# Optimization experiments

Measured on AMD Instinct MI355X. Metric: run time of the kernel, lower is better.

## Reference

```python
import jax, jax.numpy as jnp
import numpy as np

HEADS, DIM_HEAD = 8, 75            # Attention defaults in source
SCALE = DIM_HEAD ** -0.5
NUM_FOURIER = 64
PATCH = 4


def scale_norm(x, g, eps=1e-5):
    n = jnp.maximum(jnp.linalg.norm(x, axis=-1, keepdims=True), eps)
    return x / n * g


def attention(x, ctx, mask, wq, wkv, wo, bo):
    b, nq, _ = x.shape
    q = (x @ wq).reshape(b, nq, HEADS, DIM_HEAD)
    k, v = jnp.split(ctx @ wkv, 2, axis=-1)
    k = k.reshape(b, -1, HEADS, DIM_HEAD)
    v = v.reshape(b, -1, HEADS, DIM_HEAD)
    sim = jnp.einsum('bihd,bjhd->bhij', q, k) * SCALE
    if mask is not None:
        sim = jnp.where(mask[:, None, None, :], sim, -jnp.finfo(sim.dtype).max)
    a = jax.nn.softmax(sim, axis=-1)
    out = jnp.einsum('bhij,bjhd->bihd', a, v).reshape(b, nq, HEADS * DIM_HEAD)
    return out @ wo + bo


def feedforward(x, w1, b1, w2, b2):
    return jax.nn.gelu(x @ w1 + b1, approximate=False) @ w2 + b2


def fourier_encode(x, num_encodings):
    xu = x[..., None]
    scales = (2.0 ** jnp.arange(num_encodings)).astype(x.dtype)
    xs = xu / scales
    return jnp.concatenate([jnp.sin(xs), jnp.cos(xs), xu], axis=-1)


def sparsify(x, threshold=0.3):
    # x: (b, h, w, nt, c) patched volume. Fixed max_len = h*w*nt; stable sort
    # compacts kept voxels to the front in row-major (y,x,t) order, matching
    # torch.where ordering. Padded slots are zeroed and masked out.
    b, h, w, nt, c = x.shape
    N = h * w * nt
    mask = (jnp.abs(jnp.max(x, axis=-1)) > threshold).reshape(b, N)
    ys, xs, ts = jnp.meshgrid(jnp.arange(h), jnp.arange(w), jnp.arange(nt), indexing='ij')
    pos = jnp.stack([2.0 * ys / h - 1.0, 2.0 * xs / w - 1.0, 2.0 * ts / nt - 1.0], -1)
    pos = pos.reshape(N, 3).astype(x.dtype)
    order = jnp.argsort((~mask).astype(jnp.int32), axis=1)  # jax sort is stable
    mask_s = jnp.take_along_axis(mask, order, axis=1)
    pos_s = pos[order] * mask_s[..., None]
    vals_s = jnp.take_along_axis(x.reshape(b, N, c), order[..., None], axis=1) * mask_s[..., None]
    return pos_s, vals_s, mask_s


def _forward(input, latents, pos_emb,
             ca_g, ca_ctx_g, ca_q, ca_kv, ca_ow, ca_ob,
             cf_g, cf_w1, cf_b1, cf_w2, cf_b2,
             la_g, la_q, la_kv, la_ow, la_ob,
             lf_g, lf_w1, lf_b1, lf_w2, lf_b2,
             logits_w, logits_b):
    num_tbins = input.shape[0]
    x = jnp.transpose(input, (1, 3, 4, 0, 2))  # b h w t c
    b, H, W, t, c = x.shape
    p = PATCH
    x = x.reshape(b, H // p, p, W // p, p, t, c)
    x = jnp.transpose(x, (0, 1, 3, 5, 2, 4, 6)).reshape(b, H // p, W // p, t, p * p * c)
    pos, vals, mask = sparsify(x)
    enc = fourier_encode(pos, NUM_FOURIER)           # (b, N, 3, 2*nf+1)
    enc = enc.reshape(enc.shape[0], enc.shape[1], -1)
    data = jnp.concatenate([vals, enc], axis=-1)     # (b, N, input_dim)
    data = jax.lax.stop_gradient(data)               # torch builds it under no_grad
    lat = jnp.broadcast_to((latents + pos_emb)[None], (b,) + latents.shape)
    depth = ca_g.shape[0]
    for d in range(depth):
        lat = attention(scale_norm(lat, ca_g[d]), scale_norm(data, ca_ctx_g[d]), mask,
                        ca_q[d], ca_kv[d], ca_ow[d], ca_ob[d]) + lat
        lat = feedforward(scale_norm(lat, cf_g[d]), cf_w1[d], cf_b1[d], cf_w2[d], cf_b2[d]) + lat
        xn = scale_norm(lat, la_g[d])
        lat = attention(xn, xn, None, la_q[d], la_kv[d], la_ow[d], la_ob[d]) + lat
        lat = feedforward(scale_norm(lat, lf_g[d]), lf_w1[d], lf_b1[d], lf_w2[d], lf_b2[d]) + lat
    out = lat @ logits_w + logits_b                  # (b, num_latents, oc)
    n = out.shape[1] // num_tbins
    out = out.reshape(b, n, num_tbins, out.shape[-1])
    return jnp.transpose(out, (2, 0, 1, 3))          # (t, b, n, oc)


def setup_inputs() -> dict:
    key = jax.random.key(0)
    ks = jax.random.split(key, 16)
    D, LD, ID, IN, FF, NL, OC = 5, 512, 435, 600, 2048, 128, 64
    def rn(k, shape, scale=0.02):
        return jax.random.normal(k, shape, jnp.float32) * scale
    return {
        'input': jax.random.normal(ks[0], (8, 4, 3, 128, 128), jnp.float32),
        'latents': rn(ks[1], (NL, LD), 1.0),
        'pos_emb': rn(ks[2], (NL, LD), 1.0),
        'ca_g': jnp.ones((D,), jnp.float32),
        'ca_ctx_g': jnp.ones((D,), jnp.float32),
        'ca_q': rn(ks[3], (D, LD, IN)),
        'ca_kv': rn(ks[4], (D, ID, 2 * IN)),
        'ca_ow': rn(ks[5], (D, IN, LD)),
        'ca_ob': jnp.zeros((D, LD), jnp.float32),
        'cf_g': jnp.ones((D,), jnp.float32),
        'cf_w1': rn(ks[6], (D, LD, FF)),
        'cf_b1': jnp.zeros((D, FF), jnp.float32),
        'cf_w2': rn(ks[7], (D, FF, LD)),
        'cf_b2': jnp.zeros((D, LD), jnp.float32),
        'la_g': jnp.ones((D,), jnp.float32),
        'la_q': rn(ks[8], (D, LD, IN)),
        'la_kv': rn(ks[9], (D, LD, 2 * IN)),
        'la_ow': rn(ks[10], (D, IN, LD)),
        'la_ob': jnp.zeros((D, LD), jnp.float32),
        'lf_g': jnp.ones((D,), jnp.float32),
        'lf_w1': rn(ks[11], (D, LD, FF)),
        'lf_b1': jnp.zeros((D, FF), jnp.float32),
        'lf_w2': rn(ks[12], (D, FF, LD)),
        'lf_b2': jnp.zeros((D, LD), jnp.float32),
        'logits_w': rn(ks[13], (LD, OC)),
        'logits_b': jnp.zeros((OC,), jnp.float32),
    }


def reference(input, latents, pos_emb,
              ca_g, ca_ctx_g, ca_q, ca_kv, ca_ow, ca_ob,
              cf_g, cf_w1, cf_b1, cf_w2, cf_b2,
              la_g, la_q, la_kv, la_ow, la_ob,
              lf_g, lf_w1, lf_b1, lf_w2, lf_b2,
              logits_w, logits_b):
    return _forward(input, latents, pos_emb,
                    ca_g, ca_ctx_g, ca_q, ca_kv, ca_ow, ca_ob,
                    cf_g, cf_w1, cf_b1, cf_w2, cf_b2,
                    la_g, la_q, la_kv, la_ow, la_ob,
                    lf_g, lf_w1, lf_b1, lf_w2, lf_b2,
                    logits_w, logits_b)
```

## Files before the change

kernel.cpp:

```cpp
#include <hip/hip_runtime.h>
#include <math.h>

typedef unsigned short u16;
typedef long long ll;
typedef __attribute__((ext_vector_type(8))) short short8;
typedef __attribute__((ext_vector_type(4))) float f32x4;

#define TBINS 8
#define BATCH 4
#define CIN 3
#define WIMG 128
#define PC 48
#define NVOX 8192
#define ID 435
#define IDP 448
#define LD 512
#define INNER 600
#define INNERP 608
#define FFD 2048
#define NL 128
#define OC 64
#define DEPTH 5
#define HEADS 8
#define DH 75
#define DHP 96
#define BK 32
#define NCH 16
#define FCH 512
#define FKT 64

static __device__ __forceinline__ u16 f2bf(float f) {
    unsigned x = __float_as_uint(f);
    unsigned r = (x + 0x7fffu + ((x >> 16) & 1u)) >> 16;
    return (u16)r;
}
static __device__ __forceinline__ float bf2f(u16 v) {
    return __uint_as_float(((unsigned)v) << 16);
}
static __device__ __forceinline__ void gload_lds16(const u16* g, u16* l) {
    __builtin_amdgcn_global_load_lds(
        (const __attribute__((address_space(1))) unsigned int*)g,
        (__attribute__((address_space(3))) unsigned int*)l, 16, 0, 0);
}

__global__ __launch_bounds__(256) void mask_kernel(const float* __restrict__ input,
                                                   unsigned char* __restrict__ mask) {
    int idx = blockIdx.x * 256 + threadIdx.x;
    if (idx >= BATCH * NVOX) return;
    int b = idx >> 13, i = idx & (NVOX - 1);
    int tt = i & 7, wx = (i >> 3) & 31, hy = i >> 8;
    float mx = -3.4e38f;
    for (int ch = 0; ch < PC; ++ch) {
        int py = ch / 12, px = (ch / 3) & 3, cc = ch % 3;
        float v = input[((size_t)((tt * BATCH + b) * CIN + cc) << 14) +
                        (hy * 4 + py) * WIMG + (wx * 4 + px)];
        mx = fmaxf(mx, v);
    }
    mask[idx] = (fabsf(mx) > 0.3f) ? 1 : 0;
}

__global__ __launch_bounds__(64) void compact_kernel(const unsigned char* __restrict__ mask,
                                                     int* __restrict__ perm,
                                                     int* __restrict__ Kc) {
    int b = blockIdx.x, lane = threadIdx.x;
    int offs = 0;
    for (int c = 0; c < NVOX / 64; ++c) {
        int i = c * 64 + lane;
        int m = mask[(b << 13) + i];
        unsigned long long bal = __ballot(m != 0);
        int excl = __popcll(bal & ((1ull << lane) - 1ull));
        if (m) perm[(b << 13) + offs + excl] = i;
        offs += __popcll(bal);
    }
    if (lane == 0) Kc[b] = offs;
}

__global__ __launch_bounds__(256) void build_all(const float* __restrict__ input,
                                                 const int* __restrict__ perm,
                                                 const int* __restrict__ Kc,
                                                 u16* __restrict__ normed) {
    int blk = blockIdx.x;
    int b = blk >> 13, r = blk & (NVOX - 1);
    int tid = threadIdx.x;
    u16* out = normed + (size_t)blk * IDP;
    int Kb = Kc[b];
    if (r >= Kb) {
        for (int e = tid; e < IDP; e += 256) out[e] = 0;
        return;
    }
    __shared__ float row[IDP];
    __shared__ float red[256];
    int i = perm[(b << 13) + r];
    int tt = i & 7, wx = (i >> 3) & 31, hy = i >> 8;
    float pos0 = 2.f * hy / 32.f - 1.f;
    float pos1 = 2.f * wx / 32.f - 1.f;
    float pos2 = 2.f * tt / 8.f - 1.f;
    for (int e = tid; e < IDP; e += 256) {
        float v = 0.f;
        if (e < PC) {
            int py = e / 12, px = (e / 3) & 3, cc = e % 3;
            v = input[((size_t)((tt * BATCH + b) * CIN + cc) << 14) +
                      (hy * 4 + py) * WIMG + (wx * 4 + px)];
        } else if (e < ID) {
            int e2 = e - PC;
            int dim = e2 / 129, rem = e2 - dim * 129;
            float pp = (dim == 0) ? pos0 : (dim == 1 ? pos1 : pos2);
            if (rem < 64)       v = sinf(ldexpf(pp, -rem));
            else if (rem < 128) v = cosf(ldexpf(pp, -(rem - 64)));
            else                v = pp;
        }
        row[e] = v;
    }
    __syncthreads();
    float ss = 0.f;
    for (int e = tid; e < ID; e += 256) ss += row[e] * row[e];
    red[tid] = ss; __syncthreads();
    for (int s = 128; s > 0; s >>= 1) { if (tid < s) red[tid] += red[tid + s]; __syncthreads(); }
    float scale = 1.f / fmaxf(sqrtf(red[0]), 1e-5f);
    for (int e = tid; e < IDP; e += 256) out[e] = f2bf(row[e] * scale);
}

__global__ __launch_bounds__(256) void lat_init(const float* __restrict__ latents,
                                                const float* __restrict__ pos_emb,
                                                float* __restrict__ lat) {
    int idx = blockIdx.x * 256 + threadIdx.x;
    if (idx >= BATCH * NL * LD) return;
    int rem = idx & (NL * LD - 1);
    lat[idx] = latents[rem] + pos_emb[rem];
}

__global__ __launch_bounds__(256) void scale_norm_bf(const float* __restrict__ x,
                                                     u16* __restrict__ o,
                                                     const float* __restrict__ g, int gi,
                                                     int cols) {
    int rowi = blockIdx.x, tid = threadIdx.x;
    const float* xr = x + (size_t)rowi * cols;
    u16* orow = o + (size_t)rowi * cols;
    __shared__ float red[256];
    float ss = 0.f;
    for (int c = tid; c < cols; c += 256) { float v = xr[c]; ss += v * v; }
    red[tid] = ss; __syncthreads();
    for (int s = 128; s > 0; s >>= 1) { if (tid < s) red[tid] += red[tid + s]; __syncthreads(); }
    float scale = g[gi] / fmaxf(sqrtf(red[0]), 1e-5f);
    for (int c = tid; c < cols; c += 256) orow[c] = f2bf(xr[c] * scale);
}

__global__ __launch_bounds__(256) void fill_kernel(float* __restrict__ p, long long n, float v) {
    long long idx = (long long)blockIdx.x * 256 + threadIdx.x;
    if (idx < n) p[idx] = v;
}

__global__ __launch_bounds__(256) void conv_bf(const float* __restrict__ src, u16* __restrict__ dst, int n) {
    int idx = blockIdx.x * 256 + threadIdx.x;
    if (idx < n) dst[idx] = f2bf(src[idx]);
}

struct TJobs {
    const float* src[11];
    u16* dst[11];
    int R[11], C[11], Rp[11];
    int tstart[12];
    int njobs;
};
__global__ __launch_bounds__(256) void transpose_multi(TJobs J) {
    int bx = blockIdx.x;
    int j = 0;
    while (j + 1 < J.njobs && bx >= J.tstart[j + 1]) ++j;
    int lt = bx - J.tstart[j];
    int tilesX = J.Rp[j] >> 5;
    int tx = lt % tilesX, ty = lt / tilesX;
    const float* src = J.src[j];
    u16* dst = J.dst[j];
    int R = J.R[j], C = J.C[j], Rp = J.Rp[j];
    __shared__ float t[32][33];
    int bx0 = tx * 32, by0 = ty * 32;
    int ttx = threadIdx.x & 31, tty = threadIdx.x >> 5;
#pragma unroll
    for (int p = 0; p < 4; ++p) {
        int r = bx0 + tty + p * 8, c = by0 + ttx;
        t[tty + p * 8][ttx] = (r < R && c < C) ? src[(size_t)r * C + c] : 0.f;
    }
    __syncthreads();
#pragma unroll
    for (int p = 0; p < 4; ++p) {
        int c = by0 + tty + p * 8, r = bx0 + ttx;
        if (c < C && r < Rp) dst[(size_t)c * Rp + r] = f2bf(t[ttx][tty + p * 8]);
    }
}

__global__ __launch_bounds__(256) void pack_heads_u16(const u16* __restrict__ src, u16* __restrict__ dst,
                                                      int srcld) {
    int idx = blockIdx.x * 256 + threadIdx.x;
    if (idx >= BATCH * HEADS * NL * DHP) return;
    int dd = idx % DHP;
    int l = (idx / DHP) & (NL - 1);
    int bh = idx / (DHP * NL);
    int b = bh >> 3, h = bh & 7;
    dst[idx] = (dd < DH) ? src[(size_t)(b * NL + l) * srcld + h * DH + dd] : 0;
}

__global__ __launch_bounds__(256) void pack3_self(const u16* __restrict__ qkv,
                                                  u16* __restrict__ qd, u16* __restrict__ kd,
                                                  u16* __restrict__ vd) {
    const int R0 = BATCH * HEADS * NL * DHP;
    const int R2 = BATCH * HEADS * DH * NL;
    int idx = blockIdx.x * 256 + threadIdx.x;
    if (idx < 2 * R0) {
        int which = idx >= R0;
        int k = which ? idx - R0 : idx;
        int dd = k % DHP;
        int l = (k / DHP) & (NL - 1);
        int bh = k / (DHP * NL);
        int b = bh >> 3, h = bh & 7;
        u16 v = 0;
        if (dd < DH) v = qkv[(size_t)(b * NL + l) * (3 * INNER) + which * INNER + h * DH + dd];
        (which ? kd : qd)[k] = v;
    } else if (idx < 2 * R0 + R2) {
        int k = idx - 2 * R0;
        int l = k & (NL - 1);
        int dd = (k >> 7) % DH;
        int bh = k / (DH * NL);
        int b = bh >> 3, h = bh & 7;
        vd[k] = qkv[(size_t)(b * NL + l) * (3 * INNER) + 2 * INNER + h * DH + dd];
    }
}

__global__ __launch_bounds__(256) void softmax_u16(u16* __restrict__ S, int cols,
                                                   const int* __restrict__ Kc, int b0,
                                                   int rows_per_b) {
    int rowi = blockIdx.x, tid = threadIdx.x;
    u16* p = S + (size_t)rowi * cols;
    int lim = Kc ? Kc[b0 + rowi / rows_per_b] : cols;
    __shared__ float red[256];
    if (lim <= 0) { for (int j = tid; j < cols; j += 256) p[j] = 0; return; }
    float v[32];
    int nit = (lim + 255) >> 8;
    float mx = -3.4e38f;
    for (int s = 0; s < nit; ++s) {
        int j = s * 256 + tid;
        float x = (j < lim) ? bf2f(p[j]) : -3.4e38f;
        v[s] = x;
        mx = fmaxf(mx, x);
    }
    red[tid] = mx; __syncthreads();
    for (int s = 128; s > 0; s >>= 1) { if (tid < s) red[tid] = fmaxf(red[tid], red[tid + s]); __syncthreads(); }
    mx = red[0]; __syncthreads();
    float sum = 0.f;
    for (int s = 0; s < nit; ++s) {
        int j = s * 256 + tid;
        float e = (j < lim) ? expf(v[s] - mx) : 0.f;
        v[s] = e; sum += e;
    }
    red[tid] = sum; __syncthreads();
    for (int s = 128; s > 0; s >>= 1) { if (tid < s) red[tid] += red[tid + s]; __syncthreads(); }
    float inv = (red[0] > 0.f) ? 1.f / red[0] : 0.f;
    int nco = (cols + 255) >> 8;
    for (int s = 0; s < nco; ++s) {
        int j = s * 256 + tid;
        if (j < cols) p[j] = f2bf((s < nit && j < lim) ? v[s] * inv : 0.f);
    }
}

#define KS_LD 104
__global__ __launch_bounds__(256) void flash_ctx(
    const u16* __restrict__ qbf,
    const u16* __restrict__ kbf,
    const u16* __restrict__ vtg,
    const int* __restrict__ Kc,
    float* __restrict__ Opart,
    float* __restrict__ mlb,
    float scale) {
    int ch = blockIdx.x, bh = blockIdx.y;
    int b = bh >> 3;
    int lim = Kc[b];
    int v0 = ch * FCH;
    int nval = min(FCH, lim - v0);
    int tid = threadIdx.x, wv = tid >> 6, lane = tid & 63;
    int fr = lane & 15, fc = lane >> 4;
    float* Op = Opart + ((size_t)bh * NCH + ch) * (128 * 80);
    float* mlp = mlb + ((size_t)bh * NCH + ch) * 256;
    if (nval <= 0) {
        for (int i = tid; i < 128 * 80; i += 256) Op[i] = 0.f;
        for (int i = tid; i < 128; i += 256) { mlp[2 * i] = -3.4e38f; mlp[2 * i + 1] = 0.f; }
        return;
    }
    __shared__ __align__(16) u16 Ks[FKT * KS_LD];
    __shared__ __align__(16) u16 Vt[80 * 72];
    __shared__ __align__(16) u16 Ps[4 * 32 * 72];
    short8 qf[2][3];
    const u16* qb = qbf + ((size_t)bh * 128 + wv * 32) * DHP;
#pragma unroll
    for (int i = 0; i < 2; ++i)
#pragma unroll
        for (int kk = 0; kk < 3; ++kk)
            qf[i][kk] = *(const short8*)(qb + (i * 16 + fr) * DHP + kk * 32 + fc * 8);
    float m_run[2][4], l_run[2][4];
#pragma unroll
    for (int i = 0; i < 2; ++i)
#pragma unroll
        for (int r = 0; r < 4; ++r) { m_run[i][r] = -3.4e38f; l_run[i][r] = 0.f; }
    f32x4 o[2][5] = {};
    u16* Pw = Ps + wv * (32 * 72);
    int ktiles = (nval + FKT - 1) / FKT;
    for (int kt = 0; kt < ktiles; ++kt) {
        int kvox = v0 + kt * FKT;
        for (int t = 0; t < 3; ++t) {
            int idx = t * 256 + tid;
            int row = idx / 12, cc = idx - row * 12;
            short8 v = *(const short8*)(kbf + ((size_t)bh * NVOX + kvox + row) * DHP + cc * 8);
            *(short8*)(Ks + row * KS_LD + cc * 8) = v;
        }
        for (int t = 0; t < 3; ++t) {
            int idx = t * 256 + tid;
            if (idx < 640) {
                int row = idx >> 3, cc = idx & 7;
                short8 v = *(const short8*)(vtg + ((size_t)bh * DH + row) * NVOX + kvox + cc * 8);
                *(short8*)(Vt + row * 72 + cc * 8) = v;
            }
        }
        __syncthreads();
        f32x4 sc[2][4] = {};
#pragma unroll
        for (int kk = 0; kk < 3; ++kk) {
            short8 bf[4];
#pragma unroll
            for (int j = 0; j < 4; ++j)
                bf[j] = *(const short8*)(Ks + (j * 16 + fr) * KS_LD + kk * 32 + fc * 8);
#pragma unroll
            for (int i = 0; i < 2; ++i)
#pragma unroll
                for (int j = 0; j < 4; ++j)
                    sc[i][j] = __builtin_amdgcn_mfma_f32_16x16x32_bf16(qf[i][kk], bf[j], sc[i][j], 0, 0, 0);
        }
        float alpha[2][4];
#pragma unroll
        for (int i = 0; i < 2; ++i) {
#pragma unroll
            for (int r = 0; r < 4; ++r) {
                float mt = -3.4e38f;
#pragma unroll
                for (int j = 0; j < 4; ++j) {
                    int cl = kt * FKT + j * 16 + fr;
                    float s = (cl < nval) ? sc[i][j][r] * scale : -3.4e38f;
                    sc[i][j][r] = s;
                    mt = fmaxf(mt, s);
                }
                for (int sft = 1; sft < 16; sft <<= 1) mt = fmaxf(mt, __shfl_xor(mt, sft, 16));
                float mn = fmaxf(m_run[i][r], mt);
                float al = __expf(m_run[i][r] - mn);
                m_run[i][r] = mn;
                float lt = 0.f;
#pragma unroll
                for (int j = 0; j < 4; ++j) {
                    float p = __expf(sc[i][j][r] - mn);
                    sc[i][j][r] = p;
                    lt += p;
                }
                for (int sft = 1; sft < 16; sft <<= 1) lt += __shfl_xor(lt, sft, 16);
                l_run[i][r] = l_run[i][r] * al + lt;
                alpha[i][r] = al;
            }
        }
#pragma unroll
        for (int i = 0; i < 2; ++i)
#pragma unroll
            for (int j = 0; j < 4; ++j)
#pragma unroll
                for (int r = 0; r < 4; ++r)
                    Pw[(i * 16 + fc * 4 + r) * 72 + j * 16 + fr] = f2bf(sc[i][j][r]);
#pragma unroll
        for (int i = 0; i < 2; ++i)
#pragma unroll
            for (int n = 0; n < 5; ++n)
#pragma unroll
                for (int r = 0; r < 4; ++r)
                    o[i][n][r] *= alpha[i][r];
        __syncthreads();
#pragma unroll
        for (int kk = 0; kk < 2; ++kk) {
            short8 pf[2], vf[5];
#pragma unroll
            for (int i = 0; i < 2; ++i)
                pf[i] = *(const short8*)(Pw + (i * 16 + fr) * 72 + kk * 32 + fc * 8);
#pragma unroll
            for (int n = 0; n < 5; ++n)
                vf[n] = *(const short8*)(Vt + (n * 16 + fr) * 72 + kk * 32 + fc * 8);
#pragma unroll
            for (int i = 0; i < 2; ++i)
#pragma unroll
                for (int n = 0; n < 5; ++n)
                    o[i][n] = __builtin_amdgcn_mfma_f32_16x16x32_bf16(pf[i], vf[n], o[i][n], 0, 0, 0);
        }
        __syncthreads();
    }
#pragma unroll
    for (int i = 0; i < 2; ++i) {
#pragma unroll
        for (int n = 0; n < 5; ++n) {
#pragma unroll
            for (int r = 0; r < 4; ++r) {
                int row = wv * 32 + i * 16 + fc * 4 + r;
                int col = n * 16 + fr;
                Op[row * 80 + col] = o[i][n][r];
            }
        }
        if (fr == 0) {
#pragma unroll
            for (int r = 0; r < 4; ++r) {
                int row = wv * 32 + i * 16 + fc * 4 + r;
                mlp[2 * row] = m_run[i][r];
                mlp[2 * row + 1] = l_run[i][r];
            }
        }
    }
}

__global__ __launch_bounds__(128) void combine_ctx(const float* __restrict__ Opart,
                                                   const float* __restrict__ mlb,
                                                   u16* __restrict__ attn_bf) {
    int blk = blockIdx.x;
    int bh = blk >> 7, row = blk & 127;
    int b = bh >> 3, h = bh & 7;
    int tid = threadIdx.x;
    float mc[NCH], lc[NCH];
    float mstar = -3.4e38f;
    for (int c = 0; c < NCH; ++c) {
        const float* mlp = mlb + ((size_t)bh * NCH + c) * 256 + 2 * row;
        mc[c] = mlp[0]; lc[c] = mlp[1];
        mstar = fmaxf(mstar, mc[c]);
    }
    float L = 0.f;
    float wc[NCH];
    for (int c = 0; c < NCH; ++c) {
        float ww = __expf(mc[c] - mstar);
        wc[c] = ww; L += ww * lc[c];
    }
    float invL = (L > 0.f) ? 1.f / L : 0.f;
    if (tid < DH) {
        float s = 0.f;
        for (int c = 0; c < NCH; ++c)
            s += Opart[(((size_t)bh * NCH + c) * 128 + row) * 80 + tid] * wc[c];
        attn_bf[((size_t)(b * 128 + row)) * INNERP + h * DH + tid] = f2bf(s * invL);
    }
    if (h == 7 && tid >= DH && tid < DH + (INNERP - INNER))
        attn_bf[((size_t)(b * 128 + row)) * INNERP + INNER + (tid - DH)] = 0;
}

__global__ __launch_bounds__(256) void gemm_bf16(
    const u16* __restrict__ A, const u16* __restrict__ B, void* __restrict__ Dv,
    const float* __restrict__ alphaPtr, int alphaIdx, float alphaConst,
    int M, int N, int K, int lda, int ldb, int ldd, int nh,
    ll sAo, ll sAi, ll sBo, ll sBi, ll sDo, ll sDi,
    int splitK, int mode, const float* __restrict__ bias, float biasScale, int act,
    ll sKp, u16* __restrict__ kdst, u16* __restrict__ vdst) {
    __shared__ __align__(16) u16 As[128 * BK];
    __shared__ __align__(16) u16 Bs[128 * BK];
    const int tid = threadIdx.x;
    int zb = blockIdx.z / splitK, kc = blockIdx.z - zb * splitK;
    int zo = zb / nh, zi = zb - zo * nh;
    const u16* Ab = A + (size_t)zo * sAo + (size_t)zi * sAi;
    const u16* Bb = B + (size_t)zo * sBo + (size_t)zi * sBi;
    const int bm = blockIdx.x * 128, bn = blockIdx.y * 128;
    int nk = K >> 5;
    int per = (nk + splitK - 1) / splitK;
    int k0 = kc * per * BK;
    int k1 = min(K, k0 + per * BK);

    const int wv = tid >> 6, lane = tid & 63;
    const int wm = (wv & 1) << 6, wn = (wv >> 1) << 6;
    const int fr = lane & 15, fc = lane >> 4;
    f32x4 acc[4][4] = {};

    const int lr = lane >> 2, lc = (lane & 3) << 3;
    const u16* ga0 = Ab + (size_t)(bm + wv * 16 + lr) * lda + k0 + lc;
    const u16* ga1 = ga0 + (size_t)64 * lda;
    const u16* gb0 = Bb + (size_t)(bn + wv * 16 + lr) * ldb + k0 + lc;
    const u16* gb1 = gb0 + (size_t)64 * ldb;
    u16* la0 = As + (wv * 16) * BK;
    u16* la1 = As + (wv * 16 + 64) * BK;
    u16* lb0 = Bs + (wv * 16) * BK;
    u16* lb1 = Bs + (wv * 16 + 64) * BK;

    for (int kb = k0; kb < k1; kb += BK) {
        gload_lds16(ga0, la0);
        gload_lds16(ga1, la1);
        gload_lds16(gb0, lb0);
        gload_lds16(gb1, lb1);
        ga0 += BK; ga1 += BK; gb0 += BK; gb1 += BK;
        __syncthreads();
        short8 af[4], bfr[4];
#pragma unroll
        for (int i = 0; i < 4; ++i)
            af[i] = *(const short8*)(As + (wm + i * 16 + fr) * BK + fc * 8);
#pragma unroll
        for (int j = 0; j < 4; ++j)
            bfr[j] = *(const short8*)(Bs + (wn + j * 16 + fr) * BK + fc * 8);
#pragma unroll
        for (int i = 0; i < 4; ++i)
#pragma unroll
            for (int j = 0; j < 4; ++j)
                acc[i][j] = __builtin_amdgcn_mfma_f32_16x16x32_bf16(af[i], bfr[j], acc[i][j], 0, 0, 0);
        __syncthreads();
    }
    float alpha = alphaConst * (alphaPtr ? alphaPtr[alphaIdx] : 1.f);
    if (mode == 3) {
#pragma unroll
        for (int i = 0; i < 4; ++i) {
#pragma unroll
            for (int j = 0; j < 4; ++j) {
                int gn = bn + wn + j * 16 + fr;
                if (gn >= 2 * INNER) continue;
                int isV = gn >= INNER;
                int gnn = isV ? gn - INNER : gn;
                int h = gnn / DH, dd = gnn - h * DH;
                int gm0 = bm + wm + i * 16 + fc * 4;
#pragma unroll
                for (int r = 0; r < 4; ++r) {
                    int gm = gm0 + r;
                    int b2 = gm >> 13, vox = gm & (NVOX - 1);
                    u16 v = f2bf(acc[i][j][r] * alpha);
                    if (!isV) kdst[(((size_t)(b2 * 8 + h)) * NVOX + vox) * DHP + dd] = v;
                    else      vdst[((size_t)(b2 * 8 + h) * DH + dd) * NVOX + vox] = v;
                }
            }
        }
        return;
    }
    float* Db = (float*)Dv + (size_t)zo * sDo + (size_t)zi * sDi;
    u16* Du = (u16*)Dv + (size_t)zo * sDo + (size_t)zi * sDi;
    if (mode == 0) Db += (size_t)kc * sKp;
#pragma unroll
    for (int i = 0; i < 4; ++i) {
#pragma unroll
        for (int j = 0; j < 4; ++j) {
            int gn = bn + wn + j * 16 + fr;
            if (gn >= N) continue;
            float bv = bias ? bias[gn] * biasScale : 0.f;
            int gm0 = bm + wm + i * 16 + fc * 4;
#pragma unroll
            for (int r = 0; r < 4; ++r) {
                int gm = gm0 + r;
                if (gm >= M) continue;
                float v = acc[i][j][r] * alpha + bv;
                if (act) v = 0.5f * v * (1.f + erff(v * 0.70710678118654752f));
                size_t di = (size_t)gm * ldd + gn;
                if (mode == 2)      Du[di] = f2bf(v);
                else if (mode == 1) atomicAdd(&Db[di], v);
                else                Db[di] = v;
            }
        }
    }
}

__global__ __launch_bounds__(256) void reorder_kernel(const float* __restrict__ outtmp,
                                                      float* __restrict__ out) {
    int idx = blockIdx.x * 256 + threadIdx.x;
    if (idx >= TBINS * BATCH * (NL / TBINS) * OC) return;
    int oc = idx & 63, n = (idx >> 6) & 15, b = (idx >> 10) & 3, t = idx >> 12;
    out[idx] = outtmp[((size_t)(b * NL + n * TBINS + t)) * OC + oc];
}

extern "C" void kernel_launch(void* const* d_in, const int* in_sizes, int n_in,
                              void* d_out, int out_size, void* d_ws, size_t ws_size,
                              hipStream_t stream) {
    const float* input    = (const float*)d_in[0];
    const float* latents  = (const float*)d_in[1];
    const float* pos_emb  = (const float*)d_in[2];
    const float* ca_g     = (const float*)d_in[3];
    const float* ca_ctx_g = (const float*)d_in[4];
    const float* ca_q     = (const float*)d_in[5];
    const float* ca_kv    = (const float*)d_in[6];
    const float* ca_ow    = (const float*)d_in[7];
    const float* ca_ob    = (const float*)d_in[8];
    const float* cf_g     = (const float*)d_in[9];
    const float* cf_w1    = (const float*)d_in[10];
    const float* cf_b1    = (const float*)d_in[11];
    const float* cf_w2    = (const float*)d_in[12];
    const float* cf_b2    = (const float*)d_in[13];
    const float* la_g     = (const float*)d_in[14];
    const float* la_q     = (const float*)d_in[15];
    const float* la_kv    = (const float*)d_in[16];
    const float* la_ow    = (const float*)d_in[17];
    const float* la_ob    = (const float*)d_in[18];
    const float* lf_g     = (const float*)d_in[19];
    const float* lf_w1    = (const float*)d_in[20];
    const float* lf_b1    = (const float*)d_in[21];
    const float* lf_w2    = (const float*)d_in[22];
    const float* lf_b2    = (const float*)d_in[23];
    const float* logits_w = (const float*)d_in[24];
    const float* logits_b = (const float*)d_in[25];
    float* out = (float*)d_out;
    (void)ws_size; (void)n_in; (void)in_sizes; (void)out_size;

    char* w = (char*)d_ws;
    auto alloc = [&](size_t bytes) { void* p = (void*)w; w += (bytes + 255) & ~(size_t)255; return p; };
    int* perm        = (int*)alloc((size_t)BATCH * NVOX * 4);
    int* Kc          = (int*)alloc(64);
    unsigned char* mask = (unsigned char*)alloc((size_t)BATCH * NVOX);
    float* lat       = (float*)alloc((size_t)BATCH * NL * LD * 4);
    u16* latn_bf     = (u16*)alloc((size_t)BATCH * NL * LD * 2);
    u16* qg_bf       = (u16*)alloc((size_t)BATCH * NL * INNER * 2);
    u16* qkv_bf      = (u16*)alloc((size_t)BATCH * NL * 3 * INNER * 2);
    u16* attn_bf     = (u16*)alloc((size_t)BATCH * NL * INNERP * 2);
    u16* ffb_bf      = (u16*)alloc((size_t)BATCH * NL * FFD * 2);
    float* outtmp    = (float*)alloc((size_t)BATCH * NL * OC * 4);
    u16* q_bf        = (u16*)alloc((size_t)BATCH * HEADS * NL * DHP * 2);
    u16* ks_bf       = (u16*)alloc((size_t)BATCH * HEADS * NL * DHP * 2);
    u16* vs_t        = (u16*)alloc((size_t)BATCH * HEADS * DH * NL * 2);
    alloc(64 * 1024);
    u16* wq_t    = (u16*)alloc((size_t)INNER * LD * 2);
    u16* wkv_t   = (u16*)alloc((size_t)2 * INNER * IDP * 2);
    u16* wow_t   = (u16*)alloc((size_t)LD * INNERP * 2);
    u16* wf1_t   = (u16*)alloc((size_t)FFD * LD * 2);
    u16* wf2_t   = (u16*)alloc((size_t)LD * FFD * 2);
    u16* wlqkv_t = (u16*)alloc((size_t)3 * INNER * LD * 2);
    u16* wlow_t  = (u16*)alloc((size_t)LD * INNERP * 2);
    u16* wlf1_t  = (u16*)alloc((size_t)FFD * LD * 2);
    u16* wlf2_t  = (u16*)alloc((size_t)LD * FFD * 2);
    u16* wlog_t  = (u16*)alloc((size_t)OC * LD * 2);
    u16* normed  = (u16*)alloc((size_t)BATCH * NVOX * IDP * 2);
    u16* E       = (u16*)alloc((size_t)2 * 1024 * 1024);
    u16* k_bf    = (u16*)alloc((size_t)32 * NVOX * DHP * 2);
    u16* v_t     = (u16*)alloc((size_t)32 * DH * NVOX * 2);
    alloc((size_t)1 * 1024 * 1024);
    float* Opart = (float*)alloc((size_t)32 * NCH * 128 * 80 * 4);
    float* mlb   = (float*)alloc((size_t)32 * NCH * 128 * 2 * 4);

    const float scaleS = 1.0f / sqrtf((float)DH);
    const int M4 = BATCH * NL;

    auto G = [&](const u16* A, const u16* B, void* D, const float* aP, int aI, float aC,
                 int M, int N, int K, int lda, int ldb, int ldd, int nh, int nb,
                 ll sAo, ll sAi, ll sBo, ll sBi, ll sDo, ll sDi,
                 int splitK, int mode, const float* bias = nullptr, float biasScale = 1.f,
                 int act = 0, ll sKp = 0, u16* kd = nullptr, u16* vd = nullptr) {
        dim3 g((M + 127) / 128, (N + 127) / 128, nb * splitK);
        hipLaunchKernelGGL(gemm_bf16, g, dim3(256), 0, stream, A, B, D, aP, aI, aC,
                           M, N, K, lda, ldb, ldd, nh, sAo, sAi, sBo, sBi, sDo, sDi,
                           splitK, mode, bias, biasScale, act, sKp, kd, vd);
    };

    hipLaunchKernelGGL(mask_kernel, dim3((BATCH * NVOX + 255) / 256), dim3(256), 0, stream, input, mask);
    hipLaunchKernelGGL(compact_kernel, dim3(BATCH), dim3(64), 0, stream, mask, perm, Kc);
    hipLaunchKernelGGL(lat_init, dim3((BATCH * NL * LD + 255) / 256), dim3(256), 0, stream, latents, pos_emb, lat);
    hipLaunchKernelGGL(fill_kernel, dim3((((ll)32 * NVOX * DHP / 2) + 255) / 256), dim3(256), 0, stream,
                       (float*)k_bf, (ll)32 * NVOX * DHP / 2, 0.f);
    hipLaunchKernelGGL(build_all, dim3(BATCH * NVOX), dim3(256), 0, stream, input, perm, Kc, normed);

    for (int d = 0; d < DEPTH; ++d) {
        TJobs J;
        int t = 0;
        auto addJob = [&](const float* s, u16* ds, int R, int C, int Rp) {
            J.src[t] = s; J.dst[t] = ds; J.R[t] = R; J.C[t] = C; J.Rp[t] = Rp;
            J.tstart[t] = (t == 0) ? 0 : J.tstart[t - 1] +
                          (J.Rp[t - 1] >> 5) * ((J.C[t - 1] + 31) >> 5);
            ++t;
        };
        addJob(ca_q  + (size_t)d * LD * INNER,     wq_t,            LD,  INNER,     LD);
        addJob(ca_kv + (size_t)d * ID * 2 * INNER, wkv_t,           ID,  2 * INNER, IDP);
        addJob(ca_ow + (size_t)d * INNER * LD,     wow_t,           INNER, LD,      INNERP);
        addJob(cf_w1 + (size_t)d * LD * FFD,       wf1_t,           LD,  FFD,       LD);
        addJob(cf_w2 + (size_t)d * FFD * LD,       wf2_t,           FFD, LD,        FFD);
        addJob(la_q  + (size_t)d * LD * INNER,     wlqkv_t,         LD,  INNER,     LD);
        addJob(la_kv + (size_t)d * LD * 2 * INNER, wlqkv_t + (size_t)INNER * LD, LD, 2 * INNER, LD);
        addJob(la_ow + (size_t)d * INNER * LD,     wlow_t,          INNER, LD,      INNERP);
        addJob(lf_w1 + (size_t)d * LD * FFD,       wlf1_t,          LD,  FFD,       LD);
        addJob(lf_w2 + (size_t)d * FFD * LD,       wlf2_t,          FFD, LD,        FFD);
        if (d == 0) addJob(logits_w,               wlog_t,          LD,  OC,        LD);
        J.njobs = t;
        J.tstart[t] = J.tstart[t - 1] + (J.Rp[t - 1] >> 5) * ((J.C[t - 1] + 31) >> 5);
        hipLaunchKernelGGL(transpose_multi, dim3(J.tstart[t]), dim3(256), 0, stream, J);

        hipLaunchKernelGGL(scale_norm_bf, dim3(M4), dim3(256), 0, stream, lat, latn_bf, ca_g, d, LD);
        G(latn_bf, wq_t, qg_bf, nullptr, 0, 1.f, M4, INNER, LD, LD, LD, INNER, 1, 1,
          0, 0, 0, 0, 0, 0, 1, 2);
        hipLaunchKernelGGL(pack_heads_u16, dim3((BATCH * HEADS * NL * DHP + 255) / 256), dim3(256), 0, stream,
                           qg_bf, q_bf, INNER);
        G(normed, wkv_t, nullptr, ca_ctx_g, d, 1.f, BATCH * NVOX, 2 * INNER, IDP, IDP, IDP, 0, 1, 1,
          0, 0, 0, 0, 0, 0, 1, 3, nullptr, 1.f, 0, 0, k_bf, v_t);
        hipLaunchKernelGGL(flash_ctx, dim3(NCH, 32), dim3(256), 0, stream,
                           q_bf, k_bf, v_t, Kc, Opart, mlb, scaleS);
        hipLaunchKernelGGL(combine_ctx, dim3(32 * 128), dim3(128), 0, stream, Opart, mlb, attn_bf);
        G(attn_bf, wow_t, lat, nullptr, 0, 1.f, M4, LD, INNERP, INNERP, INNERP, LD, 1, 1,
          0, 0, 0, 0, 0, 0, 2, 1, ca_ob + (size_t)d * LD, 0.5f);

        hipLaunchKernelGGL(scale_norm_bf, dim3(M4), dim3(256), 0, stream, lat, latn_bf, cf_g, d, LD);
        G(latn_bf, wf1_t, ffb_bf, nullptr, 0, 1.f, M4, FFD, LD, LD, LD, FFD, 1, 1,
          0, 0, 0, 0, 0, 0, 1, 2, cf_b1 + (size_t)d * FFD, 1.f, 1);
        G(ffb_bf, wf2_t, lat, nullptr, 0, 1.f, M4, LD, FFD, FFD, FFD, LD, 1, 1,
          0, 0, 0, 0, 0, 0, 8, 1, cf_b2 + (size_t)d * LD, 0.125f);

        hipLaunchKernelGGL(scale_norm_bf, dim3(M4), dim3(256), 0, stream, lat, latn_bf, la_g, d, LD);
        G(latn_bf, wlqkv_t, qkv_bf, nullptr, 0, 1.f, M4, 3 * INNER, LD, LD, LD, 3 * INNER, 1, 1,
          0, 0, 0, 0, 0, 0, 1, 2);
        hipLaunchKernelGGL(pack3_self,
                           dim3((2 * BATCH * HEADS * NL * DHP + BATCH * HEADS * DH * NL + 255) / 256),
                           dim3(256), 0, stream, qkv_bf, q_bf, ks_bf, vs_t);
        G(q_bf, ks_bf, E, nullptr, 0, scaleS, NL, NL, DHP, DHP, DHP, NL, 32, 32,
          0, (ll)NL * DHP, 0, (ll)NL * DHP, 0, (ll)NL * NL, 1, 2);
        hipLaunchKernelGGL(softmax_u16, dim3(BATCH * HEADS * NL), dim3(256), 0, stream,
                           E, NL, (const int*)nullptr, 0, HEADS * NL);
        G(E, vs_t, attn_bf, nullptr, 0, 1.f, NL, DH, NL, NL, NL, INNERP, 8, 32,
          (ll)HEADS * NL * NL, (ll)NL * NL, (ll)HEADS * DH * NL, (ll)DH * NL,
          (ll)NL * INNERP, (ll)DH, 1, 2);
        G(attn_bf, wlow_t, lat, nullptr, 0, 1.f, M4, LD, INNERP, INNERP, INNERP, LD, 1, 1,
          0, 0, 0, 0, 0, 0, 2, 1, la_ob + (size_t)d * LD, 0.5f);

        hipLaunchKernelGGL(scale_norm_bf, dim3(M4), dim3(256), 0, stream, lat, latn_bf, lf_g, d, LD);
        G(latn_bf, wlf1_t, ffb_bf, nullptr, 0, 1.f, M4, FFD, LD, LD, LD, FFD, 1, 1,
          0, 0, 0, 0, 0, 0, 1, 2, lf_b1 + (size_t)d * FFD, 1.f, 1);
        G(ffb_bf, wlf2_t, lat, nullptr, 0, 1.f, M4, LD, FFD, FFD, FFD, LD, 1, 1,
          0, 0, 0, 0, 0, 0, 8, 1, lf_b2 + (size_t)d * LD, 0.125f);
    }

    hipLaunchKernelGGL(conv_bf, dim3((M4 * LD + 255) / 256), dim3(256), 0, stream, lat, latn_bf, M4 * LD);
    hipLaunchKernelGGL(fill_kernel, dim3((M4 * OC + 255) / 256), dim3(256), 0, stream,
                       outtmp, (ll)M4 * OC, 0.f);
    G(latn_bf, wlog_t, outtmp, nullptr, 0, 1.f, M4, OC, LD, LD, LD, OC, 1, 1,
      0, 0, 0, 0, 0, 0, 4, 1, logits_b, 0.25f);
    hipLaunchKernelGGL(reorder_kernel, dim3((TBINS * BATCH * (NL / TBINS) * OC + 255) / 256), dim3(256), 0,
                       stream, outtmp, out);
}
```

Baseline: 2.268 ms.

## Pad weight columns per head so GEMMs emit head-padded layouts directly

Weight transposes now scatter Q, KV and QKV columns into head-padded (96-wide) slots, so the projection GEMMs write a per-head-padded layout. That removes the separate pack kernels and the scatter epilogue that wrote K and transposed V. flash_ctx now reads K and V straight from the interleaved KV buffer and transposes V into LDS itself, and the self-attention QK GEMM reads strided Q/K in place. The logits GEMM writes the final reordered output with atomics, which drops the reorder kernel. In exchange, the cross-attention KV GEMM writes a wider padded output, and the in-kernel V transpose in LDS may cause bank conflicts.

```diff
diff --git a/kernel.cpp b/kernel.cpp
--- a/kernel.cpp
+++ b/kernel.cpp
@@ -28,6 +28,9 @@
 #define NCH 16
 #define FCH 512
 #define FKT 64
+#define KVLD 1536
+#define QLD 768
+#define QKVLD 2304
 
 static __device__ __forceinline__ u16 f2bf(float f) {
     unsigned x = __float_as_uint(f);
@@ -158,7 +161,7 @@
 struct TJobs {
     const float* src[11];
     u16* dst[11];
-    int R[11], C[11], Rp[11];
+    int R[11], C[11], Rp[11], flag[11];
     int tstart[12];
     int njobs;
 };
@@ -171,7 +174,7 @@
     int tx = lt % tilesX, ty = lt / tilesX;
     const float* src = J.src[j];
     u16* dst = J.dst[j];
-    int R = J.R[j], C = J.C[j], Rp = J.Rp[j];
+    int R = J.R[j], C = J.C[j], Rp = J.Rp[j], fl = J.flag[j];
     __shared__ float t[32][33];
     int bx0 = tx * 32, by0 = ty * 32;
     int ttx = threadIdx.x & 31, tty = threadIdx.x >> 5;
@@ -184,45 +187,24 @@
 #pragma unroll
     for (int p = 0; p < 4; ++p) {
         int c = by0 + tty + p * 8, r = bx0 + ttx;
-        if (c < C && r < Rp) dst[(size_t)c * Rp + r] = f2bf(t[ttx][tty + p * 8]);
-    }
-}
-
-__global__ __launch_bounds__(256) void pack_heads_u16(const u16* __restrict__ src, u16* __restrict__ dst,
-                                                      int srcld) {
+        if (c < C && r < Rp) {
+            int cp = c;
+            if (fl == 1)      cp = (c / 75) * 96 + c % 75;
+            else if (fl == 2) { int sec = c / 600, rem = c - sec * 600;
+                                cp = sec * 768 + (rem / 75) * 96 + rem % 75; }
+            dst[(size_t)cp * Rp + r] = f2bf(t[ttx][tty + p * 8]);
+        }
+    }
+}
+
+__global__ __launch_bounds__(256) void pack_vt_self(const u16* __restrict__ qkvs, u16* __restrict__ vt) {
     int idx = blockIdx.x * 256 + threadIdx.x;
-    if (idx >= BATCH * HEADS * NL * DHP) return;
-    int dd = idx % DHP;
-    int l = (idx / DHP) & (NL - 1);
-    int bh = idx / (DHP * NL);
+    if (idx >= BATCH * HEADS * DH * NL) return;
+    int l = idx & (NL - 1);
+    int dd = (idx >> 7) % DH;
+    int bh = idx / (DH * NL);
     int b = bh >> 3, h = bh & 7;
-    dst[idx] = (dd < DH) ? src[(size_t)(b * NL + l) * srcld + h * DH + dd] : 0;
-}
-
-__global__ __launch_bounds__(256) void pack3_self(const u16* __restrict__ qkv,
-                                                  u16* __restrict__ qd, u16* __restrict__ kd,
-                                                  u16* __restrict__ vd) {
-    const int R0 = BATCH * HEADS * NL * DHP;
-    const int R2 = BATCH * HEADS * DH * NL;
-    int idx = blockIdx.x * 256 + threadIdx.x;
-    if (idx < 2 * R0) {
-        int which = idx >= R0;
-        int k = which ? idx - R0 : idx;
-        int dd = k % DHP;
-        int l = (k / DHP) & (NL - 1);
-        int bh = k / (DHP * NL);
-        int b = bh >> 3, h = bh & 7;
-        u16 v = 0;
-        if (dd < DH) v = qkv[(size_t)(b * NL + l) * (3 * INNER) + which * INNER + h * DH + dd];
-        (which ? kd : qd)[k] = v;
-    } else if (idx < 2 * R0 + R2) {
-        int k = idx - 2 * R0;
-        int l = k & (NL - 1);
-        int dd = (k >> 7) % DH;
-        int bh = k / (DH * NL);
-        int b = bh >> 3, h = bh & 7;
-        vd[k] = qkv[(size_t)(b * NL + l) * (3 * INNER) + 2 * INNER + h * DH + dd];
-    }
+    vt[idx] = qkvs[(size_t)(b * NL + l) * QKVLD + 2 * QLD + h * DHP + dd];
 }
 
 __global__ __launch_bounds__(256) void softmax_u16(u16* __restrict__ S, int cols,
@@ -263,15 +245,14 @@
 
 #define KS_LD 104
 __global__ __launch_bounds__(256) void flash_ctx(
-    const u16* __restrict__ qbf,
-    const u16* __restrict__ kbf,
-    const u16* __restrict__ vtg,
+    const u16* __restrict__ qg,
+    const u16* __restrict__ kvn,
     const int* __restrict__ Kc,
     float* __restrict__ Opart,
     float* __restrict__ mlb,
     float scale) {
     int ch = blockIdx.x, bh = blockIdx.y;
-    int b = bh >> 3;
+    int b = bh >> 3, h = bh & 7;
     int lim = Kc[b];
     int v0 = ch * FCH;
     int nval = min(FCH, lim - v0);
@@ -287,13 +268,15 @@
     __shared__ __align__(16) u16 Ks[FKT * KS_LD];
     __shared__ __align__(16) u16 Vt[80 * 72];
     __shared__ __align__(16) u16 Ps[4 * 32 * 72];
+    const u16* kbase = kvn + ((size_t)b * NVOX) * KVLD + h * DHP;
+    const u16* vbase = kbase + QLD;
     short8 qf[2][3];
-    const u16* qb = qbf + ((size_t)bh * 128 + wv * 32) * DHP;
+    const u16* qb = qg + ((size_t)(b * NL) + wv * 32) * QLD + h * DHP;
 #pragma unroll
     for (int i = 0; i < 2; ++i)
 #pragma unroll
         for (int kk = 0; kk < 3; ++kk)
-            qf[i][kk] = *(const short8*)(qb + (i * 16 + fr) * DHP + kk * 32 + fc * 8);
+            qf[i][kk] = *(const short8*)(qb + (size_t)(i * 16 + fr) * QLD + kk * 32 + fc * 8);
     float m_run[2][4], l_run[2][4];
 #pragma unroll
     for (int i = 0; i < 2; ++i)
@@ -307,15 +290,17 @@
         for (int t = 0; t < 3; ++t) {
             int idx = t * 256 + tid;
             int row = idx / 12, cc = idx - row * 12;
-            short8 v = *(const short8*)(kbf + ((size_t)bh * NVOX + kvox + row) * DHP + cc * 8);
+            short8 v = *(const short8*)(kbase + (size_t)(kvox + row) * KVLD + cc * 8);
             *(short8*)(Ks + row * KS_LD + cc * 8) = v;
         }
         for (int t = 0; t < 3; ++t) {
             int idx = t * 256 + tid;
             if (idx < 640) {
-                int row = idx >> 3, cc = idx & 7;
-                short8 v = *(const short8*)(vtg + ((size_t)bh * DH + row) * NVOX + kvox + cc * 8);
-                *(short8*)(Vt + row * 72 + cc * 8) = v;
+                int row = idx / 10, c8 = idx - row * 10;
+                short8 v = *(const short8*)(vbase + (size_t)(kvox + row) * KVLD + c8 * 8);
+#pragma unroll
+                for (int e = 0; e < 8; ++e)
+                    Vt[(c8 * 8 + e) * 72 + row] = (u16)v[e];
             }
         }
         __syncthreads();
@@ -396,14 +381,12 @@
 #pragma unroll
     for (int i = 0; i < 2; ++i) {
 #pragma unroll
-        for (int n = 0; n < 5; ++n) {
+        for (int n = 0; n < 5; ++n)
 #pragma unroll
             for (int r = 0; r < 4; ++r) {
                 int row = wv * 32 + i * 16 + fc * 4 + r;
-                int col = n * 16 + fr;
-                Op[row * 80 + col] = o[i][n][r];
+                Op[row * 80 + n * 16 + fr] = o[i][n][r];
             }
-        }
         if (fr == 0) {
 #pragma unroll
             for (int r = 0; r < 4; ++r) {
@@ -451,8 +434,7 @@
     const float* __restrict__ alphaPtr, int alphaIdx, float alphaConst,
     int M, int N, int K, int lda, int ldb, int ldd, int nh,
     ll sAo, ll sAi, ll sBo, ll sBi, ll sDo, ll sDi,
-    int splitK, int mode, const float* __restrict__ bias, float biasScale, int act,
-    ll sKp, u16* __restrict__ kdst, u16* __restrict__ vdst) {
+    int splitK, int mode, const float* __restrict__ bias, float biasScale, int act) {
     __shared__ __align__(16) u16 As[128 * BK];
     __shared__ __align__(16) u16 Bs[128 * BK];
     const int tid = threadIdx.x;
@@ -503,32 +485,30 @@
         __syncthreads();
     }
     float alpha = alphaConst * (alphaPtr ? alphaPtr[alphaIdx] : 1.f);
-    if (mode == 3) {
-#pragma unroll
-        for (int i = 0; i < 4; ++i) {
+    if (mode == 6) {
+        float* Do = (float*)Dv;
+#pragma unroll
+        for (int i = 0; i < 4; ++i)
 #pragma unroll
             for (int j = 0; j < 4; ++j) {
                 int gn = bn + wn + j * 16 + fr;
-                if (gn >= 2 * INNER) continue;
-                int isV = gn >= INNER;
-                int gnn = isV ? gn - INNER : gn;
-                int h = gnn / DH, dd = gnn - h * DH;
+                if (gn >= N) continue;
+                float bv = bias ? bias[gn] * biasScale : 0.f;
                 int gm0 = bm + wm + i * 16 + fc * 4;
 #pragma unroll
                 for (int r = 0; r < 4; ++r) {
                     int gm = gm0 + r;
-                    int b2 = gm >> 13, vox = gm & (NVOX - 1);
-                    u16 v = f2bf(acc[i][j][r] * alpha);
-                    if (!isV) kdst[(((size_t)(b2 * 8 + h)) * NVOX + vox) * DHP + dd] = v;
-                    else      vdst[((size_t)(b2 * 8 + h) * DH + dd) * NVOX + vox] = v;
+                    if (gm >= M) continue;
+                    int b = gm >> 7, l = gm & 127;
+                    int tt = l & 7, nn = l >> 3;
+                    atomicAdd(&Do[(((size_t)(tt * BATCH + b)) * 16 + nn) * 64 + gn],
+                              acc[i][j][r] * alpha + bv);
                 }
             }
-        }
         return;
     }
     float* Db = (float*)Dv + (size_t)zo * sDo + (size_t)zi * sDi;
     u16* Du = (u16*)Dv + (size_t)zo * sDo + (size_t)zi * sDi;
-    if (mode == 0) Db += (size_t)kc * sKp;
 #pragma unroll
     for (int i = 0; i < 4; ++i) {
 #pragma unroll
@@ -544,20 +524,11 @@
                 float v = acc[i][j][r] * alpha + bv;
                 if (act) v = 0.5f * v * (1.f + erff(v * 0.70710678118654752f));
                 size_t di = (size_t)gm * ldd + gn;
-                if (mode == 2)      Du[di] = f2bf(v);
-                else if (mode == 1) atomicAdd(&Db[di], v);
-                else                Db[di] = v;
+                if (mode == 2) Du[di] = f2bf(v);
+                else           atomicAdd(&Db[di], v);
             }
         }
     }
-}
-
-__global__ __launch_bounds__(256) void reorder_kernel(const float* __restrict__ outtmp,
-                                                      float* __restrict__ out) {
-    int idx = blockIdx.x * 256 + threadIdx.x;
-    if (idx >= TBINS * BATCH * (NL / TBINS) * OC) return;
-    int oc = idx & 63, n = (idx >> 6) & 15, b = (idx >> 10) & 3, t = idx >> 12;
-    out[idx] = outtmp[((size_t)(b * NL + n * TBINS + t)) * OC + oc];
 }
 
 extern "C" void kernel_launch(void* const* d_in, const int* in_sizes, int n_in,
@@ -599,30 +570,27 @@
     unsigned char* mask = (unsigned char*)alloc((size_t)BATCH * NVOX);
     float* lat       = (float*)alloc((size_t)BATCH * NL * LD * 4);
     u16* latn_bf     = (u16*)alloc((size_t)BATCH * NL * LD * 2);
-    u16* qg_bf       = (u16*)alloc((size_t)BATCH * NL * INNER * 2);
-    u16* qkv_bf      = (u16*)alloc((size_t)BATCH * NL * 3 * INNER * 2);
+    u16* qg          = (u16*)alloc((size_t)BATCH * NL * QLD * 2);
+    u16* qkvs        = (u16*)alloc((size_t)BATCH * NL * QKVLD * 2);
     u16* attn_bf     = (u16*)alloc((size_t)BATCH * NL * INNERP * 2);
     u16* ffb_bf      = (u16*)alloc((size_t)BATCH * NL * FFD * 2);
-    float* outtmp    = (float*)alloc((size_t)BATCH * NL * OC * 4);
-    u16* q_bf        = (u16*)alloc((size_t)BATCH * HEADS * NL * DHP * 2);
-    u16* ks_bf       = (u16*)alloc((size_t)BATCH * HEADS * NL * DHP * 2);
     u16* vs_t        = (u16*)alloc((size_t)BATCH * HEADS * DH * NL * 2);
     alloc(64 * 1024);
-    u16* wq_t    = (u16*)alloc((size_t)INNER * LD * 2);
-    u16* wkv_t   = (u16*)alloc((size_t)2 * INNER * IDP * 2);
+    u16* wqp_t   = (u16*)alloc((size_t)QLD * LD * 2);
+    u16* wkv_t   = (u16*)alloc((size_t)KVLD * IDP * 2);
+    u16* wlqkv_t = (u16*)alloc((size_t)QKVLD * LD * 2);
+    size_t padw_f32 = ((size_t)QLD * LD + (size_t)KVLD * IDP + (size_t)QKVLD * LD) / 2;
     u16* wow_t   = (u16*)alloc((size_t)LD * INNERP * 2);
     u16* wf1_t   = (u16*)alloc((size_t)FFD * LD * 2);
     u16* wf2_t   = (u16*)alloc((size_t)LD * FFD * 2);
-    u16* wlqkv_t = (u16*)alloc((size_t)3 * INNER * LD * 2);
     u16* wlow_t  = (u16*)alloc((size_t)LD * INNERP * 2);
     u16* wlf1_t  = (u16*)alloc((size_t)FFD * LD * 2);
     u16* wlf2_t  = (u16*)alloc((size_t)LD * FFD * 2);
     u16* wlog_t  = (u16*)alloc((size_t)OC * LD * 2);
     u16* normed  = (u16*)alloc((size_t)BATCH * NVOX * IDP * 2);
     u16* E       = (u16*)alloc((size_t)2 * 1024 * 1024);
-    u16* k_bf    = (u16*)alloc((size_t)32 * NVOX * DHP * 2);
-    u16* v_t     = (u16*)alloc((size_t)32 * DH * NVOX * 2);
-    alloc((size_t)1 * 1024 * 1024);
+    u16* kvn     = (u16*)alloc((size_t)BATCH * NVOX * KVLD * 2);
+    alloc((size_t)64 * 1024);
     float* Opart = (float*)alloc((size_t)32 * NCH * 128 * 80 * 4);
     float* mlb   = (float*)alloc((size_t)32 * NCH * 128 * 2 * 4);
 
@@ -633,53 +601,51 @@
                  int M, int N, int K, int lda, int ldb, int ldd, int nh, int nb,
                  ll sAo, ll sAi, ll sBo, ll sBi, ll sDo, ll sDi,
                  int splitK, int mode, const float* bias = nullptr, float biasScale = 1.f,
-                 int act = 0, ll sKp = 0, u16* kd = nullptr, u16* vd = nullptr) {
+                 int act = 0) {
         dim3 g((M + 127) / 128, (N + 127) / 128, nb * splitK);
         hipLaunchKernelGGL(gemm_bf16, g, dim3(256), 0, stream, A, B, D, aP, aI, aC,
                            M, N, K, lda, ldb, ldd, nh, sAo, sAi, sBo, sBi, sDo, sDi,
-                           splitK, mode, bias, biasScale, act, sKp, kd, vd);
+                           splitK, mode, bias, biasScale, act);
     };
 
     hipLaunchKernelGGL(mask_kernel, dim3((BATCH * NVOX + 255) / 256), dim3(256), 0, stream, input, mask);
     hipLaunchKernelGGL(compact_kernel, dim3(BATCH), dim3(64), 0, stream, mask, perm, Kc);
     hipLaunchKernelGGL(lat_init, dim3((BATCH * NL * LD + 255) / 256), dim3(256), 0, stream, latents, pos_emb, lat);
-    hipLaunchKernelGGL(fill_kernel, dim3((((ll)32 * NVOX * DHP / 2) + 255) / 256), dim3(256), 0, stream,
-                       (float*)k_bf, (ll)32 * NVOX * DHP / 2, 0.f);
+    hipLaunchKernelGGL(fill_kernel, dim3(((ll)padw_f32 + 255) / 256), dim3(256), 0, stream,
+                       (float*)wqp_t, (ll)padw_f32, 0.f);
     hipLaunchKernelGGL(build_all, dim3(BATCH * NVOX), dim3(256), 0, stream, input, perm, Kc, normed);
 
     for (int d = 0; d < DEPTH; ++d) {
         TJobs J;
         int t = 0;
-        auto addJob = [&](const float* s, u16* ds, int R, int C, int Rp) {
-            J.src[t] = s; J.dst[t] = ds; J.R[t] = R; J.C[t] = C; J.Rp[t] = Rp;
+        auto addJob = [&](const float* s, u16* ds, int R, int C, int Rp, int fl) {
+            J.src[t] = s; J.dst[t] = ds; J.R[t] = R; J.C[t] = C; J.Rp[t] = Rp; J.flag[t] = fl;
             J.tstart[t] = (t == 0) ? 0 : J.tstart[t - 1] +
                           (J.Rp[t - 1] >> 5) * ((J.C[t - 1] + 31) >> 5);
             ++t;
         };
-        addJob(ca_q  + (size_t)d * LD * INNER,     wq_t,            LD,  INNER,     LD);
-        addJob(ca_kv + (size_t)d * ID * 2 * INNER, wkv_t,           ID,  2 * INNER, IDP);
-        addJob(ca_ow + (size_t)d * INNER * LD,     wow_t,           INNER, LD,      INNERP);
-        addJob(cf_w1 + (size_t)d * LD * FFD,       wf1_t,           LD,  FFD,       LD);
-        addJob(cf_w2 + (size_t)d * FFD * LD,       wf2_t,           FFD, LD,        FFD);
-        addJob(la_q  + (size_t)d * LD * INNER,     wlqkv_t,         LD,  INNER,     LD);
-        addJob(la_kv + (size_t)d * LD * 2 * INNER, wlqkv_t + (size_t)INNER * LD, LD, 2 * INNER, LD);
-        addJob(la_ow + (size_t)d * INNER * LD,     wlow_t,          INNER, LD,      INNERP);
-        addJob(lf_w1 + (size_t)d * LD * FFD,       wlf1_t,          LD,  FFD,       LD);
-        addJob(lf_w2 + (size_t)d * FFD * LD,       wlf2_t,          FFD, LD,        FFD);
-        if (d == 0) addJob(logits_w,               wlog_t,          LD,  OC,        LD);
+        addJob(ca_q  + (size_t)d * LD * INNER,     wqp_t,   LD,  INNER,     LD,     1);
+        addJob(ca_kv + (size_t)d * ID * 2 * INNER, wkv_t,   ID,  2 * INNER, IDP,    2);
+        addJob(ca_ow + (size_t)d * INNER * LD,     wow_t,   INNER, LD,      INNERP, 0);
+        addJob(cf_w1 + (size_t)d * LD * FFD,       wf1_t,   LD,  FFD,       LD,     0);
+        addJob(cf_w2 + (size_t)d * FFD * LD,       wf2_t,   FFD, LD,        FFD,    0);
+        addJob(la_q  + (size_t)d * LD * INNER,     wlqkv_t, LD,  INNER,     LD,     1);
+        addJob(la_kv + (size_t)d * LD * 2 * INNER, wlqkv_t + (size_t)QLD * LD, LD, 2 * INNER, LD, 2);
+        addJob(la_ow + (size_t)d * INNER * LD,     wlow_t,  INNER, LD,      INNERP, 0);
+        addJob(lf_w1 + (size_t)d * LD * FFD,       wlf1_t,  LD,  FFD,       LD,     0);
+        addJob(lf_w2 + (size_t)d * FFD * LD,       wlf2_t,  FFD, LD,        FFD,    0);
+        if (d == 0) addJob(logits_w,               wlog_t,  LD,  OC,        LD,     0);
         J.njobs = t;
         J.tstart[t] = J.tstart[t - 1] + (J.Rp[t - 1] >> 5) * ((J.C[t - 1] + 31) >> 5);
         hipLaunchKernelGGL(transpose_multi, dim3(J.tstart[t]), dim3(256), 0, stream, J);
 
         hipLaunchKernelGGL(scale_norm_bf, dim3(M4), dim3(256), 0, stream, lat, latn_bf, ca_g, d, LD);
-        G(latn_bf, wq_t, qg_bf, nullptr, 0, 1.f, M4, INNER, LD, LD, LD, INNER, 1, 1,
+        G(latn_bf, wqp_t, qg, nullptr, 0, 1.f, M4, QLD, LD, LD, LD, QLD, 1, 1,
           0, 0, 0, 0, 0, 0, 1, 2);
-        hipLaunchKernelGGL(pack_heads_u16, dim3((BATCH * HEADS * NL * DHP + 255) / 256), dim3(256), 0, stream,
-                           qg_bf, q_bf, INNER);
-        G(normed, wkv_t, nullptr, ca_ctx_g, d, 1.f, BATCH * NVOX, 2 * INNER, IDP, IDP, IDP, 0, 1, 1,
-          0, 0, 0, 0, 0, 0, 1, 3, nullptr, 1.f, 0, 0, k_bf, v_t);
+        G(normed, wkv_t, kvn, ca_ctx_g, d, 1.f, BATCH * NVOX, KVLD, IDP, IDP, IDP, KVLD, 1, 1,
+          0, 0, 0, 0, 0, 0, 1, 2);
         hipLaunchKernelGGL(flash_ctx, dim3(NCH, 32), dim3(256), 0, stream,
-                           q_bf, k_bf, v_t, Kc, Opart, mlb, scaleS);
+                           qg, kvn, Kc, Opart, mlb, scaleS);
         hipLaunchKernelGGL(combine_ctx, dim3(32 * 128), dim3(128), 0, stream, Opart, mlb, attn_bf);
         G(attn_bf, wow_t, lat, nullptr, 0, 1.f, M4, LD, INNERP, INNERP, INNERP, LD, 1, 1,
           0, 0, 0, 0, 0, 0, 2, 1, ca_ob + (size_t)d * LD, 0.5f);
@@ -691,13 +657,13 @@
           0, 0, 0, 0, 0, 0, 8, 1, cf_b2 + (size_t)d * LD, 0.125f);
 
         hipLaunchKernelGGL(scale_norm_bf, dim3(M4), dim3(256), 0, stream, lat, latn_bf, la_g, d, LD);
-        G(latn_bf, wlqkv_t, qkv_bf, nullptr, 0, 1.f, M4, 3 * INNER, LD, LD, LD, 3 * INNER, 1, 1,
+        G(latn_bf, wlqkv_t, qkvs, nullptr, 0, 1.f, M4, QKVLD, LD, LD, LD, QKVLD, 1, 1,
           0, 0, 0, 0, 0, 0, 1, 2);
-        hipLaunchKernelGGL(pack3_self,
-                           dim3((2 * BATCH * HEADS * NL * DHP + BATCH * HEADS * DH * NL + 255) / 256),
-                           dim3(256), 0, stream, qkv_bf, q_bf, ks_bf, vs_t);
-        G(q_bf, ks_bf, E, nullptr, 0, scaleS, NL, NL, DHP, DHP, DHP, NL, 32, 32,
-          0, (ll)NL * DHP, 0, (ll)NL * DHP, 0, (ll)NL * NL, 1, 2);
+        hipLaunchKernelGGL(pack_vt_self, dim3((BATCH * HEADS * DH * NL + 255) / 256), dim3(256), 0, stream,
+                           qkvs, vs_t);
+        G(qkvs, qkvs + QLD, E, nullptr, 0, scaleS, NL, NL, DHP, QKVLD, QKVLD, NL, 8, 32,
+          (ll)NL * QKVLD, (ll)DHP, (ll)NL * QKVLD, (ll)DHP,
+          (ll)HEADS * NL * NL, (ll)NL * NL, 1, 2);
         hipLaunchKernelGGL(softmax_u16, dim3(BATCH * HEADS * NL), dim3(256), 0, stream,
                            E, NL, (const int*)nullptr, 0, HEADS * NL);
         G(E, vs_t, attn_bf, nullptr, 0, 1.f, NL, DH, NL, NL, NL, INNERP, 8, 32,
@@ -714,10 +680,8 @@
     }
 
     hipLaunchKernelGGL(conv_bf, dim3((M4 * LD + 255) / 256), dim3(256), 0, stream, lat, latn_bf, M4 * LD);
-    hipLaunchKernelGGL(fill_kernel, dim3((M4 * OC + 255) / 256), dim3(256), 0, stream,
-                       outtmp, (ll)M4 * OC, 0.f);
-    G(latn_bf, wlog_t, outtmp, nullptr, 0, 1.f, M4, OC, LD, LD, LD, OC, 1, 1,
-      0, 0, 0, 0, 0, 0, 4, 1, logits_b, 0.25f);
-    hipLaunchKernelGGL(reorder_kernel, dim3((TBINS * BATCH * (NL / TBINS) * OC + 255) / 256), dim3(256), 0,
-                       stream, outtmp, out);
-}
+    hipLaunchKernelGGL(fill_kernel, dim3((TBINS * BATCH * 16 * OC + 255) / 256), dim3(256), 0, stream,
+                       out, (ll)TBINS * BATCH * 16 * OC, 0.f);
+    G(latn_bf, wlog_t, out, nullptr, 0, 1.f, M4, OC, LD, LD, LD, 0, 1, 1,
+      0, 0, 0, 0, 0, 0, 4, 6, logits_b, 0.25f);
+}
```

Result: faster. 2.131 ms (-6.0%).
